# Performance work log

Hardware: AMD Instinct MI355X
Metric: run time of the kernel (lower is better)

The kernel has to match this reference:

```python
import jax, jax.numpy as jnp
import numpy as np


def setup_inputs() -> dict:
    key = jax.random.key(0)
    k0, k1, k2, k3 = jax.random.split(key, 4)
    B, L, D, H = 8, 4096, 300, 128  # batch, leaves (power of 2), embed dim, hidden
    x = jax.random.normal(k0, (B, L, D), jnp.float32)
    W_leaf = jax.random.normal(k1, (D, 2 * H), jnp.float32) * (1.0 / np.sqrt(D))
    b_leaf = jnp.zeros((2 * H,), jnp.float32)
    W_l = jax.random.normal(k2, (H, 5 * H), jnp.float32) * (1.0 / np.sqrt(H))
    W_r = jax.random.normal(k3, (H, 5 * H), jnp.float32) * (1.0 / np.sqrt(H))
    b = jnp.zeros((5 * H,), jnp.float32)
    return {"x": x, "W_leaf": W_leaf, "b_leaf": b_leaf, "W_l": W_l, "W_r": W_r, "b": b}


def reference(x, W_leaf, b_leaf, W_l, W_r, b):
    """Binary TreeLSTM over a complete tree: leaves -> root.

    x: [B, L, D] leaf embeddings, L a power of 2.
    Leaf transform: linear projection split into (h, c) (SPINN-style).
    REDUCE: 5-gate child-sum-of-two composition.
    Returns root hidden state: [B, H].
    """
    H = W_l.shape[0]
    hc = x @ W_leaf + b_leaf                     # [B, L, 2H]
    h, c = hc[..., :H], hc[..., H:]
    levels = int(np.log2(x.shape[1]))
    for _ in range(levels):                      # level-batched tree reduction
        h_l, h_r = h[:, 0::2], h[:, 1::2]        # [B, n/2, H]
        c_l, c_r = c[:, 0::2], c[:, 1::2]
        gates = h_l @ W_l + h_r @ W_r + b        # [B, n/2, 5H]
        i, fl, fr, o, g = jnp.split(gates, 5, axis=-1)
        c = (jax.nn.sigmoid(fl) * c_l
             + jax.nn.sigmoid(fr) * c_r
             + jax.nn.sigmoid(i) * jnp.tanh(g))
        h = jax.nn.sigmoid(o) * jnp.tanh(c)
    return h[:, 0]                               # root hidden state [B, H]
```

## Files before the change

### kernel.cpp

```cpp
#include <hip/hip_runtime.h>
#include <hip/hip_bf16.h>
#include <math.h>


typedef __attribute__((ext_vector_type(8))) short bfrag8;
typedef __attribute__((ext_vector_type(4))) float f32x4;
typedef __attribute__((ext_vector_type(4))) short s16x4;

__device__ __forceinline__ float sigf(float x) { return 1.0f / (1.0f + __expf(-x)); }
__device__ __forceinline__ short f2bf(float f) {
    __hip_bfloat16 h = __float2bfloat16(f);
    return *reinterpret_cast<short*>(&h);
}
#define GLDS(gp, lp) __builtin_amdgcn_global_load_lds( \
    (const __attribute__((address_space(1))) void*)(gp), \
    (__attribute__((address_space(3))) void*)(lp), 16, 0, 0)

__global__ __launch_bounds__(256) void reorder_kernel(
    const float* __restrict__ W_l, const float* __restrict__ W_r,
    const float* __restrict__ W_leaf,
    short* __restrict__ Wcat_ch, short* __restrict__ Wleaf_ch)
{
    int idx = blockIdx.x * 256 + threadIdx.x;
    if (idx < 163840) {
        int n = idx >> 8, k = idx & 255;
        float v = (k < 128) ? W_l[k * 640 + n] : W_r[(k - 128) * 640 + n];
        Wcat_ch[(((size_t)(k >> 3)) * 640 + n) * 8 + (k & 7)] = f2bf(v);
        return;
    }
    idx -= 163840;
    if (idx < 81920) {
        int n = idx / 320, k = idx - n * 320;
        short v = (k < 300) ? f2bf(W_leaf[k * 256 + n]) : (short)0;
        Wleaf_ch[(((size_t)(k >> 3)) * 256 + n) * 8 + (k & 7)] = v;
    }
}

__global__ __launch_bounds__(256) void convx_kernel(
    const float* __restrict__ x, short* __restrict__ xbf)
{
    __shared__ short Ls[64 * 328];
    const int tid = threadIdx.x;
    const int R0 = blockIdx.x * 64;
    for (int i = tid; i < 64 * 75; i += 256) {
        int r = i / 75, q = i - r * 75;
        f32x4 v = *(const f32x4*)(x + (size_t)(R0 + r) * 300 + q * 4);
        s16x4 o;
        #pragma unroll
        for (int t = 0; t < 4; ++t) o[t] = f2bf(v[t]);
        *(s16x4*)(Ls + r * 328 + q * 4) = o;
    }
    for (int i = tid; i < 64 * 20; i += 256) {
        int r = i / 20, q = i - r * 20;
        Ls[r * 328 + 300 + q] = 0;
    }
    __syncthreads();
    for (int i = tid; i < 40 * 64; i += 256) {
        int c = i >> 6, r = i & 63;
        bfrag8 v = *(const bfrag8*)(Ls + r * 328 + c * 8);
        *(bfrag8*)(xbf + ((size_t)c * 32768 + R0 + r) * 8) = v;
    }
}

__global__ __launch_bounds__(256) void leaf_kernel(
    const short* __restrict__ A, const short* __restrict__ B,
    const float* __restrict__ bleaf,
    short* __restrict__ hD,
    float* __restrict__ cD)
{
    __shared__ short Als[8 * 128 * 8];
    __shared__ short Bls[8 * 128 * 8];
    const int tid  = threadIdx.x;
    const int w    = tid >> 6, lane = tid & 63;
    const int quad = lane >> 4, l16 = lane & 15;
    const int mBlk = blockIdx.x * 128, nBlk = blockIdx.y * 128;
    const int waveM = (w >> 1) * 64, waveN = (w & 1) * 64;

    f32x4 acc[4][4] = {};

    for (int k0 = 0; k0 < 40; k0 += 8) {
        #pragma unroll
        for (int q = 0; q < 4; ++q) {
            int rr = w * 4 + q, cl = rr >> 1, rh = rr & 1;
            GLDS(A + ((size_t)(k0 + cl) * 32768 + mBlk + rh * 64 + lane) * 8,
                 (char*)Als + rr * 1024);
            GLDS(B + ((size_t)(k0 + cl) * 256 + nBlk + rh * 64 + lane) * 8,
                 (char*)Bls + rr * 1024);
        }
        __syncthreads();
        #pragma unroll
        for (int ks = 0; ks < 2; ++ks) {
            int ca = ks * 4 + quad;
            bfrag8 af[4], bf[4];
            #pragma unroll
            for (int i = 0; i < 4; ++i)
                af[i] = *(const bfrag8*)(Als + (ca * 128 + waveM + i * 16 + l16) * 8);
            #pragma unroll
            for (int jn = 0; jn < 4; ++jn)
                bf[jn] = *(const bfrag8*)(Bls + (ca * 128 + waveN + jn * 16 + l16) * 8);
            #pragma unroll
            for (int i = 0; i < 4; ++i)
                #pragma unroll
                for (int jn = 0; jn < 4; ++jn)
                    acc[i][jn] = __builtin_amdgcn_mfma_f32_16x16x32_bf16(
                                     af[i], bf[jn], acc[i][jn], 0, 0, 0);
        }
        __syncthreads();
    }

    #pragma unroll
    for (int i = 0; i < 4; ++i) {
        int row0 = mBlk + waveM + i * 16 + quad * 4;
        #pragma unroll
        for (int jn = 0; jn < 4; ++jn) {
            int col = nBlk + waveN + jn * 16 + l16;
            float bv = bleaf[col];
            #pragma unroll
            for (int rg = 0; rg < 4; ++rg) {
                float v = acc[i][jn][rg] + bv;
                int m = row0 + rg;
                if (nBlk == 0) {
                    int hc = col;
                    hD[(((size_t)((m & 1) * 16 + (hc >> 3))) * 16384 + (m >> 1)) * 8
                       + (hc & 7)] = f2bf(v);
                } else {
                    cD[(size_t)m * 128 + (col - 128)] = v;
                }
            }
        }
    }
}

__global__ __launch_bounds__(256, 2) void level_ws_kernel(
    const short* __restrict__ A,
    const float* __restrict__ cprev,
    const short* __restrict__ Wch,
    const float* __restrict__ bias,
    short* __restrict__ hout, float* __restrict__ cout,
    int M, float* __restrict__ out_final)
{
    __shared__ short Als[32 * 64 * 8];
    const int tid  = threadIdx.x;
    const int w    = tid >> 6, lane = tid & 63;
    const int quad = lane >> 4, l16 = lane & 15;
    const int j  = blockIdx.y;
    const int tb = blockIdx.x * 64;
    const int h  = j * 16 + l16;

    {
        int row = tb + lane; if (row >= M) row = 0;
        #pragma unroll
        for (int s = 0; s < 8; ++s)
            GLDS(A + ((size_t)(s * 4 + w) * M + row) * 8,
                 (char*)Als + (s * 4 + w) * 1024);
    }

    bfrag8 Wfr[5][8];
    #pragma unroll
    for (int g = 0; g < 5; ++g)
        #pragma unroll
        for (int s = 0; s < 8; ++s)
            Wfr[g][s] = *(const bfrag8*)(Wch + ((size_t)(s * 4 + quad) * 640
                                                + g * 128 + h) * 8);
    const float bi  = bias[h],       bfl = bias[128 + h], bfr_ = bias[256 + h];
    const float bo  = bias[384 + h], bg  = bias[512 + h];

    __syncthreads();

    f32x4 acc[5] = {};
    #pragma unroll
    for (int s = 0; s < 8; ++s) {
        bfrag8 af = *(const bfrag8*)(Als + ((s * 4 + quad) * 64 + w * 16 + l16) * 8);
        #pragma unroll
        for (int g = 0; g < 5; ++g)
            acc[g] = __builtin_amdgcn_mfma_f32_16x16x32_bf16(af, Wfr[g][s], acc[g], 0, 0, 0);
    }

    const int Mn = M >> 1;
    #pragma unroll
    for (int rg = 0; rg < 4; ++rg) {
        int m = tb + w * 16 + quad * 4 + rg;
        if (m < M) {
            float gi  = acc[0][rg] + bi;
            float gfl = acc[1][rg] + bfl;
            float gfr = acc[2][rg] + bfr_;
            float go  = acc[3][rg] + bo;
            float gg  = acc[4][rg] + bg;
            float cl  = cprev[(size_t)(2 * m) * 128 + h];
            float cr  = cprev[(size_t)(2 * m + 1) * 128 + h];
            float cn  = sigf(gfl) * cl + sigf(gfr) * cr + sigf(gi) * tanhf(gg);
            float hn  = sigf(go) * tanhf(cn);
            if (out_final) {
                out_final[(size_t)m * 128 + h] = hn;
            } else {
                hout[(((size_t)((m & 1) * 16 + (h >> 3))) * Mn + (m >> 1)) * 8
                     + (h & 7)] = f2bf(hn);
                cout[(size_t)m * 128 + h] = cn;
            }
        }
    }
}

extern "C" void kernel_launch(void* const* d_in, const int* in_sizes, int n_in,
                              void* d_out, int out_size, void* d_ws, size_t ws_size,
                              hipStream_t stream)
{
    const float* x      = (const float*)d_in[0];
    const float* W_leaf = (const float*)d_in[1];
    const float* b_leaf = (const float*)d_in[2];
    const float* W_l    = (const float*)d_in[3];
    const float* W_r    = (const float*)d_in[4];
    const float* b      = (const float*)d_in[5];
    float* out = (float*)d_out;

    char* p = (char*)d_ws;
    short* xbf   = (short*)p; p += (size_t)40 * 32768 * 16;
    short* hA    = (short*)p; p += (size_t)32 * 16384 * 16 + 1024;
    short* hB    = (short*)p; p += (size_t)32 * 8192 * 16 + 1024;
    float* c0    = (float*)p; p += (size_t)32768 * 128 * 4;
    float* c1    = (float*)p; p += (size_t)16384 * 128 * 4;
    short* WcatC = (short*)p; p += (size_t)32 * 640 * 16;
    short* WlfC  = (short*)p; p += (size_t)40 * 256 * 16;

    reorder_kernel<<<960, 256, 0, stream>>>(W_l, W_r, W_leaf, WcatC, WlfC);
    convx_kernel<<<512, 256, 0, stream>>>(x, xbf);
    leaf_kernel<<<dim3(256, 2), 256, 0, stream>>>(xbf, WlfC, b_leaf, hA, c0);

    const short* hin = hA; const float* cin = c0;
    int M = 16384;
    for (int lev = 1; lev <= 12; ++lev) {
        short* ho = (lev & 1) ? hB : hA;
        float* co = (lev & 1) ? c1 : c0;
        float* of = (lev == 12) ? out : nullptr;
        level_ws_kernel<<<dim3((M + 63) / 64, 8), 256, 0, stream>>>(
            hin, cin, WcatC, b, ho, co, M, of);
        hin = ho; cin = co;
        M >>= 1;
    }
}
```

Before: 207.4 us.

## Double-buffer leaf GEMM, stage weights in LDS, fuse last four levels into one kernel

The leaf GEMM now double-buffers its A/B LDS tiles so the next K-slice loads while MFMAs run, and it drops one barrier per iteration. The level kernel stages its weight slice in LDS through async global-to-LDS loads instead of scattered per-lane global loads. The last four tree levels (M=64..8) run in a single one-block tail kernel that keeps h and c in shared memory, replacing four tiny launches. The tail runs on one CU, so those levels get little parallelism in exchange for less launch overhead and latency.

```diff
diff --git a/kernel.cpp b/kernel.cpp
--- a/kernel.cpp
+++ b/kernel.cpp
@@ -62,14 +62,14 @@
     }
 }
 
-__global__ __launch_bounds__(256) void leaf_kernel(
+__global__ __launch_bounds__(256, 2) void leaf_kernel(
     const short* __restrict__ A, const short* __restrict__ B,
     const float* __restrict__ bleaf,
     short* __restrict__ hD,
     float* __restrict__ cD)
 {
-    __shared__ short Als[8 * 128 * 8];
-    __shared__ short Bls[8 * 128 * 8];
+    __shared__ short Als[2][8 * 128 * 8];
+    __shared__ short Bls[2][8 * 128 * 8];
     const int tid  = threadIdx.x;
     const int w    = tid >> 6, lane = tid & 63;
     const int quad = lane >> 4, l16 = lane & 15;
@@ -78,26 +78,34 @@
 
     f32x4 acc[4][4] = {};
 
-    for (int k0 = 0; k0 < 40; k0 += 8) {
+    auto stage = [&](int k0, int buf) {
         #pragma unroll
         for (int q = 0; q < 4; ++q) {
             int rr = w * 4 + q, cl = rr >> 1, rh = rr & 1;
             GLDS(A + ((size_t)(k0 + cl) * 32768 + mBlk + rh * 64 + lane) * 8,
-                 (char*)Als + rr * 1024);
+                 (char*)Als[buf] + rr * 1024);
             GLDS(B + ((size_t)(k0 + cl) * 256 + nBlk + rh * 64 + lane) * 8,
-                 (char*)Bls + rr * 1024);
+                 (char*)Bls[buf] + rr * 1024);
         }
+    };
+
+    stage(0, 0);
+    #pragma unroll
+    for (int s = 0; s < 5; ++s) {
         __syncthreads();
+        if (s < 4) stage((s + 1) * 8, (s + 1) & 1);
+        const short* Ab = Als[s & 1];
+        const short* Bb = Bls[s & 1];
         #pragma unroll
         for (int ks = 0; ks < 2; ++ks) {
             int ca = ks * 4 + quad;
             bfrag8 af[4], bf[4];
             #pragma unroll
             for (int i = 0; i < 4; ++i)
-                af[i] = *(const bfrag8*)(Als + (ca * 128 + waveM + i * 16 + l16) * 8);
+                af[i] = *(const bfrag8*)(Ab + (ca * 128 + waveM + i * 16 + l16) * 8);
             #pragma unroll
             for (int jn = 0; jn < 4; ++jn)
-                bf[jn] = *(const bfrag8*)(Bls + (ca * 128 + waveN + jn * 16 + l16) * 8);
+                bf[jn] = *(const bfrag8*)(Bb + (ca * 128 + waveN + jn * 16 + l16) * 8);
             #pragma unroll
             for (int i = 0; i < 4; ++i)
                 #pragma unroll
@@ -105,7 +113,6 @@
                     acc[i][jn] = __builtin_amdgcn_mfma_f32_16x16x32_bf16(
                                      af[i], bf[jn], acc[i][jn], 0, 0, 0);
         }
-        __syncthreads();
     }
 
     #pragma unroll
@@ -139,6 +146,7 @@
     short* __restrict__ hout, float* __restrict__ cout,
     int M, float* __restrict__ out_final)
 {
+    __shared__ short Wlds[32 * 80 * 8];
     __shared__ short Als[32 * 64 * 8];
     const int tid  = threadIdx.x;
     const int w    = tid >> 6, lane = tid & 63;
@@ -147,6 +155,15 @@
     const int tb = blockIdx.x * 64;
     const int h  = j * 16 + l16;
 
+    #pragma unroll
+    for (int q = 0; q < 10; ++q) {
+        int r = w * 10 + q;
+        int u = r * 64 + lane;
+        int c = u / 80, np = u - c * 80;
+        int g = np >> 4, hh = np & 15;
+        GLDS(Wch + ((size_t)c * 640 + g * 128 + j * 16 + hh) * 8,
+             (char*)Wlds + r * 1024);
+    }
     {
         int row = tb + lane; if (row >= M) row = 0;
         #pragma unroll
@@ -154,18 +171,16 @@
             GLDS(A + ((size_t)(s * 4 + w) * M + row) * 8,
                  (char*)Als + (s * 4 + w) * 1024);
     }
+    __syncthreads();
 
     bfrag8 Wfr[5][8];
     #pragma unroll
     for (int g = 0; g < 5; ++g)
         #pragma unroll
         for (int s = 0; s < 8; ++s)
-            Wfr[g][s] = *(const bfrag8*)(Wch + ((size_t)(s * 4 + quad) * 640
-                                                + g * 128 + h) * 8);
+            Wfr[g][s] = *(const bfrag8*)(Wlds + (((s * 4 + quad) * 80) + g * 16 + l16) * 8);
     const float bi  = bias[h],       bfl = bias[128 + h], bfr_ = bias[256 + h];
     const float bo  = bias[384 + h], bg  = bias[512 + h];
-
-    __syncthreads();
 
     f32x4 acc[5] = {};
     #pragma unroll
@@ -201,6 +216,95 @@
     }
 }
 
+__global__ __launch_bounds__(512, 2) void tail_kernel(
+    const short* __restrict__ A9g,
+    const float* __restrict__ c9in,
+    const short* __restrict__ Wch, const float* __restrict__ bias,
+    float* __restrict__ out)
+{
+    __shared__ short A9[32 * 64 * 8];
+    __shared__ short A10[32 * 32 * 8];
+    __shared__ short A11[32 * 16 * 8];
+    __shared__ short A12[32 * 16 * 8];
+    __shared__ float c9[64 * 128];
+    __shared__ float c10[32 * 128];
+    __shared__ float c11[16 * 128];
+    const int tid  = threadIdx.x;
+    const int w    = tid >> 6, lane = tid & 63;
+    const int quad = lane >> 4, l16 = lane & 15;
+    const int h    = w * 16 + l16;
+
+    #pragma unroll
+    for (int q = 0; q < 4; ++q) {
+        int r = w * 4 + q;
+        GLDS(A9g + ((size_t)r * 64 + lane) * 8, (char*)A9 + r * 1024);
+    }
+    bfrag8 Wfr[5][8];
+    #pragma unroll
+    for (int g = 0; g < 5; ++g)
+        #pragma unroll
+        for (int s = 0; s < 8; ++s)
+            Wfr[g][s] = *(const bfrag8*)(Wch + ((size_t)(s * 4 + quad) * 640
+                                                + g * 128 + h) * 8);
+    const float bi  = bias[h],       bfl = bias[128 + h], bfr_ = bias[256 + h];
+    const float bo  = bias[384 + h], bg  = bias[512 + h];
+    __syncthreads();
+
+#define TAIL_LEVEL(MM, AINARR, CREAD, STORE)                                          \
+    {                                                                                 \
+        const int NT = ((MM) + 15) >> 4;                                              \
+        for (int t0 = 0; t0 < NT; t0 += 2) {                                          \
+            const int np = (NT - t0 < 2) ? (NT - t0) : 2;                             \
+            f32x4 acc[2][5] = {};                                                     \
+            for (int s = 0; s < 8; ++s) {                                             \
+                for (int tt = 0; tt < np; ++tt) {                                     \
+                    int rowl = (t0 + tt) * 16 + l16;                                  \
+                    if (rowl >= (MM)) rowl = (MM) - 1;                                \
+                    bfrag8 af = *(const bfrag8*)(AINARR                               \
+                                  + ((s * 4 + quad) * (MM) + rowl) * 8);              \
+                    for (int g = 0; g < 5; ++g)                                       \
+                        acc[tt][g] = __builtin_amdgcn_mfma_f32_16x16x32_bf16(         \
+                                         af, Wfr[g][s], acc[tt][g], 0, 0, 0);         \
+                }                                                                     \
+            }                                                                         \
+            for (int tt = 0; tt < np; ++tt)                                           \
+                for (int rg = 0; rg < 4; ++rg) {                                      \
+                    int m = (t0 + tt) * 16 + quad * 4 + rg;                           \
+                    if (m < (MM)) {                                                   \
+                        float gi  = acc[tt][0][rg] + bi;                              \
+                        float gfl = acc[tt][1][rg] + bfl;                             \
+                        float gfr = acc[tt][2][rg] + bfr_;                            \
+                        float go  = acc[tt][3][rg] + bo;                              \
+                        float gg  = acc[tt][4][rg] + bg;                              \
+                        float cl, cr; CREAD;                                          \
+                        float cn = sigf(gfl) * cl + sigf(gfr) * cr                    \
+                                 + sigf(gi) * tanhf(gg);                              \
+                        float hn = sigf(go) * tanhf(cn);                              \
+                        STORE;                                                        \
+                    }                                                                 \
+                }                                                                     \
+        }                                                                             \
+        __syncthreads();                                                              \
+    }
+
+    TAIL_LEVEL(64, A9,
+        { cl = c9in[(size_t)(2 * m) * 128 + h]; cr = c9in[(size_t)(2 * m + 1) * 128 + h]; },
+        { A10[(((m & 1) * 16 + (h >> 3)) * 32 + (m >> 1)) * 8 + (h & 7)] = f2bf(hn);
+          c9[m * 128 + h] = cn; })
+    TAIL_LEVEL(32, A10,
+        { cl = c9[(2 * m) * 128 + h]; cr = c9[(2 * m + 1) * 128 + h]; },
+        { A11[(((m & 1) * 16 + (h >> 3)) * 16 + (m >> 1)) * 8 + (h & 7)] = f2bf(hn);
+          c10[m * 128 + h] = cn; })
+    TAIL_LEVEL(16, A11,
+        { cl = c10[(2 * m) * 128 + h]; cr = c10[(2 * m + 1) * 128 + h]; },
+        { A12[(((m & 1) * 16 + (h >> 3)) * 8 + (m >> 1)) * 8 + (h & 7)] = f2bf(hn);
+          c11[m * 128 + h] = cn; })
+    TAIL_LEVEL(8, A12,
+        { cl = c11[(2 * m) * 128 + h]; cr = c11[(2 * m + 1) * 128 + h]; },
+        { out[(size_t)m * 128 + h] = hn; })
+#undef TAIL_LEVEL
+}
+
 extern "C" void kernel_launch(void* const* d_in, const int* in_sizes, int n_in,
                               void* d_out, int out_size, void* d_ws, size_t ws_size,
                               hipStream_t stream)
@@ -228,13 +332,13 @@
 
     const short* hin = hA; const float* cin = c0;
     int M = 16384;
-    for (int lev = 1; lev <= 12; ++lev) {
+    for (int lev = 1; lev <= 8; ++lev) {
         short* ho = (lev & 1) ? hB : hA;
         float* co = (lev & 1) ? c1 : c0;
-        float* of = (lev == 12) ? out : nullptr;
         level_ws_kernel<<<dim3((M + 63) / 64, 8), 256, 0, stream>>>(
-            hin, cin, WcatC, b, ho, co, M, of);
+            hin, cin, WcatC, b, ho, co, M, nullptr);
         hin = ho; cin = co;
         M >>= 1;
     }
-}
+    tail_kernel<<<1, 512, 0, stream>>>(hin, cin, WcatC, b, out);
+}
```

New measurement: 209.0 us. About the same (+0.8%).
